# Optimization experiments

Hardware: AMD Instinct MI355X
Metric: run time of the kernel (lower is better)

## Reference

```python
import jax, jax.numpy as jnp
import numpy as np

GAMMA, LMBD, EPS = 0.99, 0.95, 0.2
T, D, H, A = 262144, 128, 256, 8


def _mlp_gauss(x, W1, b1, Wmu, bmu, Wlv, blv):
    h = jnp.tanh(x @ W1 + b1)
    return h @ Wmu + bmu, h @ Wlv + blv  # mu, logvar: [T, A]


def _critic(x, Wc1, bc1, Wc2, bc2):
    h = jnp.tanh(x @ Wc1 + bc1)
    return h @ Wc2 + bc2  # [T, 1]


def setup_inputs() -> dict:
    key = jax.random.key(0)
    ks = jax.random.split(key, 12)
    s = 0.05  # small init scale for stable exp()/ratio
    return {
        "state": jax.random.normal(ks[0], (T, D), jnp.float32),
        "next_state": jax.random.normal(ks[1], (T, D), jnp.float32),
        "action": jax.random.normal(ks[2], (T, A), jnp.float32),
        "beta_log_prob": jax.random.normal(ks[3], (T, A), jnp.float32) * 0.1,
        "reward": jax.random.normal(ks[4], (T,), jnp.float32),
        "W1": jax.random.normal(ks[5], (D, H), jnp.float32) * s,
        "b1": jnp.zeros((H,), jnp.float32),
        "Wmu": jax.random.normal(ks[6], (H, A), jnp.float32) * s,
        "bmu": jnp.zeros((A,), jnp.float32),
        "Wlv": jax.random.normal(ks[7], (H, A), jnp.float32) * s,
        "blv": jnp.zeros((A,), jnp.float32),
        "Wc1": jax.random.normal(ks[8], (D, H), jnp.float32) * s,
        "bc1": jnp.zeros((H,), jnp.float32),
        "Wc2": jax.random.normal(ks[9], (H, 1), jnp.float32) * s,
        "bc2": jnp.zeros((1,), jnp.float32),
    }


def reference(state, next_state, action, beta_log_prob, reward,
              W1, b1, Wmu, bmu, Wlv, blv, Wc1, bc1, Wc2, bc2):
    # critic values
    value = _critic(state, Wc1, bc1, Wc2, bc2)            # [T, 1]
    v0 = value[:, 0]                                       # [T]
    v1 = _critic(next_state, Wc1, bc1, Wc2, bc2)[:, 0]     # [T]

    # GAE: reverse recurrence gae_t = delta_t + gamma*lambda*gae_{t+1}
    delta = reward + GAMMA * v1 - v0                       # [T]

    def step(g, d):
        g = d + GAMMA * LMBD * g
        return g, g

    _, gae_rev = jax.lax.scan(step, jnp.float32(0.0), delta[::-1])
    # torch code rebuilds each gae into a fresh Tensor -> returns are detached
    ret = jax.lax.stop_gradient(gae_rev[::-1][:, None])    # [T, 1]

    advantage = ret - value                                # [T, 1] (grad via value)
    a_hat = (advantage - advantage.mean()) / (jnp.std(advantage, ddof=1) + 1e-7)

    # pi log-prob of actions under Normal(mu, sqrt(exp(logvar)))
    mu, logvar = _mlp_gauss(state, W1, b1, Wmu, bmu, Wlv, blv)  # [T, A]
    log_2pi = jnp.float32(np.log(2.0 * np.pi))
    pi_lp = -0.5 * ((action - mu) ** 2) * jnp.exp(-logvar) - 0.5 * logvar - 0.5 * log_2pi

    ratio = jnp.exp(jnp.sum(pi_lp - jax.lax.stop_gradient(beta_log_prob),
                            axis=1, keepdims=True))        # [T, 1]

    actor_loss = -jnp.sum(jnp.minimum(ratio * a_hat,
                                      jnp.clip(ratio, 1.0 - EPS, 1.0 + EPS) * a_hat))
    critic_loss = jnp.sum(advantage ** 2)
    return actor_loss + critic_loss
```

## Files before the change

### kernel.cpp

```cpp
#include <hip/hip_runtime.h>

#define T_N   262144
#define D_IN  128
#define H_HID 256
#define A_DIM 8
#define GAMMA 0.99f
#define LMBD  0.95f
#define EPS_C 0.2f
#define C_GL  0.9405f
#define W16C  0.37474927f
#define CHUNK 4096
#define NCHUNK 64
#define HALF_LOG_2PI 0.9189385332f

typedef __attribute__((ext_vector_type(8))) short short8;
typedef __attribute__((ext_vector_type(4))) float f32x4;

__device__ __forceinline__ unsigned short f2bf(float f) {
  unsigned int u = __float_as_uint(f);
  u += 0x7FFFu + ((u >> 16) & 1u);
  return (unsigned short)(u >> 16);
}
__device__ __forceinline__ float bf2f(unsigned short h) {
  return __uint_as_float(((unsigned int)h) << 16);
}
__device__ __forceinline__ float fast_tanh(float x) {
  x = fminf(10.f, fmaxf(-10.f, x));
  float e = __expf(2.f * x);
  return 1.f - 2.f * __builtin_amdgcn_rcpf(e + 1.f);
}

__global__ __launch_bounds__(256) void k_prep(
    const float* __restrict__ Wc1, const float* __restrict__ W1,
    const float* __restrict__ Wc2, const float* __restrict__ Wmu,
    const float* __restrict__ Wlv,
    unsigned short* __restrict__ Wc1T, unsigned short* __restrict__ W1T,
    unsigned short* __restrict__ H0, unsigned short* __restrict__ H1) {
  int i = blockIdx.x * 256 + threadIdx.x;
  if (i < 32768) {
    int n = i >> 7, k = i & 127;
    Wc1T[i] = f2bf(Wc1[k * 256 + n]);
  } else if (i < 65536) {
    int j = i - 32768; int n = j >> 7, k = j & 127;
    W1T[j] = f2bf(W1[k * 256 + n]);
  } else if (i < 69632) {
    int j = i - 65536; int h = j >> 8, n = j & 255;
    H0[j] = (h == 0) ? f2bf(Wc2[n]) : (unsigned short)0;
  } else if (i < 73728) {
    int j = i - 69632; int h = j >> 8, n = j & 255;
    H1[j] = (h < 8) ? f2bf(Wmu[n * 8 + h]) : f2bf(Wlv[n * 8 + (h - 8)]);
  }
}

__global__ __launch_bounds__(256) void k_main(
    const float* __restrict__ state, const float* __restrict__ next_state,
    const float* __restrict__ action, const float* __restrict__ beta_lp,
    const unsigned short* __restrict__ Wc1T, const unsigned short* __restrict__ W1T,
    const unsigned short* __restrict__ H0, const unsigned short* __restrict__ H1,
    const float* __restrict__ bc1, const float* __restrict__ b1,
    const float* __restrict__ bc2, const float* __restrict__ bmu,
    const float* __restrict__ blv,
    float* __restrict__ v0out, float* __restrict__ v1out,
    float* __restrict__ ratio) {
  const int job = blockIdx.y;
  const int r0  = blockIdx.x * 64;
  const int tid = threadIdx.x;
  const int lane = tid & 63;
  const int wv   = tid >> 6;
  const int c    = lane & 15;
  const int quad = lane >> 4;

  __shared__ unsigned short sh_x[64 * 136];
  __shared__ unsigned short sh_h[64 * 264];
  __shared__ unsigned short sh_wh[16 * 264];
  __shared__ float sh_hb[64 * 16];

  const float* X = (job == 1) ? next_state : state;
  const unsigned short* WT = (job == 2) ? W1T : Wc1T;
  const float* bias = (job == 2) ? b1 : bc1;
  const unsigned short* HW = (job == 2) ? H1 : H0;

  {
    const float4* Xv = (const float4*)(X + r0 * D_IN);
#pragma unroll
    for (int it = 0; it < 8; ++it) {
      int f4 = tid + it * 256;
      int row = f4 >> 5, c4 = f4 & 31;
      float4 v = Xv[f4];
      ushort4 u;
      u.x = f2bf(v.x); u.y = f2bf(v.y); u.z = f2bf(v.z); u.w = f2bf(v.w);
      *(ushort4*)(&sh_x[row * 136 + c4 * 4]) = u;
    }
#pragma unroll
    for (int it = 0; it < 16; ++it) {
      int j = tid + it * 256;
      sh_wh[(j >> 8) * 264 + (j & 255)] = HW[j];
    }
  }
  __syncthreads();

  short8 bfrag[4][4];
  float bias_c[4];
#pragma unroll
  for (int ct = 0; ct < 4; ++ct) {
    int n = wv * 64 + ct * 16 + c;
    bias_c[ct] = bias[n];
#pragma unroll
    for (int ki = 0; ki < 4; ++ki)
      bfrag[ct][ki] = *(const short8*)(WT + n * 128 + ki * 32 + quad * 8);
  }

#pragma unroll
  for (int rt = 0; rt < 4; ++rt) {
    f32x4 acc[4];
#pragma unroll
    for (int ct = 0; ct < 4; ++ct) acc[ct] = (f32x4){0.f, 0.f, 0.f, 0.f};
#pragma unroll
    for (int ki = 0; ki < 4; ++ki) {
      short8 a = *(const short8*)(&sh_x[(rt * 16 + c) * 136 + ki * 32 + quad * 8]);
#pragma unroll
      for (int ct = 0; ct < 4; ++ct)
        acc[ct] = __builtin_amdgcn_mfma_f32_16x16x32_bf16(a, bfrag[ct][ki], acc[ct], 0, 0, 0);
    }
#pragma unroll
    for (int ct = 0; ct < 4; ++ct) {
      int col = wv * 64 + ct * 16 + c;
#pragma unroll
      for (int r = 0; r < 4; ++r) {
        int row = rt * 16 + quad * 4 + r;
        sh_h[row * 264 + col] = f2bf(fast_tanh(acc[ct][r] + bias_c[ct]));
      }
    }
  }
  __syncthreads();

  {
    f32x4 acc2 = (f32x4){0.f, 0.f, 0.f, 0.f};
#pragma unroll
    for (int ki = 0; ki < 8; ++ki) {
      short8 a2 = *(const short8*)(&sh_wh[c * 264 + ki * 32 + quad * 8]);
      short8 b2 = *(const short8*)(&sh_h[(wv * 16 + c) * 264 + ki * 32 + quad * 8]);
      acc2 = __builtin_amdgcn_mfma_f32_16x16x32_bf16(a2, b2, acc2, 0, 0, 0);
    }
    *((f32x4*)&sh_hb[(wv * 16 + c) * 16 + quad * 4]) = acc2;
  }
  __syncthreads();

  if (tid < 64) {
    int s = tid, t = r0 + s;
    if (job == 0) {
      v0out[t] = sh_hb[s * 16] + bc2[0];
    } else if (job == 1) {
      v1out[t] = sh_hb[s * 16] + bc2[0];
    } else {
      float slp = 0.f;
#pragma unroll
      for (int a = 0; a < A_DIM; ++a) {
        float mu = sh_hb[s * 16 + a] + bmu[a];
        float lv = sh_hb[s * 16 + 8 + a] + blv[a];
        float ac = action[t * A_DIM + a];
        float bl = beta_lp[t * A_DIM + a];
        float d = ac - mu;
        slp += -0.5f * d * d * __expf(-lv) - 0.5f * lv - HALF_LOG_2PI - bl;
      }
      ratio[t] = __expf(slp);
    }
  }
}

__global__ __launch_bounds__(256) void k_delta(
    const float* __restrict__ reward, const float* __restrict__ v0,
    const float* __restrict__ v1, float* __restrict__ delta,
    float* __restrict__ chunkS) {
  int j = blockIdx.x, k = threadIdx.x;
  int base = j * CHUNK + k * 16;
  float s = 0.f, wgt = 1.f;
#pragma unroll
  for (int i = 0; i < 16; ++i) {
    float d = reward[base + i] + GAMMA * v1[base + i] - v0[base + i];
    delta[base + i] = d;
    s += wgt * d;
    wgt *= C_GL;
  }
  __shared__ float red[256];
  red[k] = __powf(W16C, (float)k) * s;
  __syncthreads();
  for (int off = 128; off > 0; off >>= 1) {
    if (k < off) red[k] += red[k + off];
    __syncthreads();
  }
  if (k == 0) chunkS[j] = red[0];
}

__global__ void k_carry(const float* __restrict__ chunkS, float* __restrict__ carry) {
  if (threadIdx.x == 0) {
    float g = 0.f;
    for (int j = NCHUNK - 1; j >= 0; --j) {
      carry[j] = g;
      g = chunkS[j] + 0.0f * g;
    }
  }
}

__global__ __launch_bounds__(256) void k_gae(
    const float* __restrict__ delta, const float* __restrict__ value,
    const float* __restrict__ carry, float* __restrict__ adv,
    float* __restrict__ accs) {
  int j = blockIdx.x, k = threadIdx.x;
  int base = j * CHUNK + k * 16;
  float d[16];
  float s = 0.f, wgt = 1.f;
#pragma unroll
  for (int i = 0; i < 16; ++i) {
    d[i] = delta[base + i];
    s += wgt * d[i];
    wgt *= C_GL;
  }
  __shared__ float Ss[256], Sw[256];
  Ss[k] = s; Sw[k] = W16C;
  __syncthreads();
  for (int dd = 1; dd < 256; dd <<= 1) {
    bool has = (k + dd) < 256;
    float ns = 0.f, nw = 0.f;
    if (has) { ns = Ss[k] + Sw[k] * Ss[k + dd]; nw = Sw[k] * Sw[k + dd]; }
    __syncthreads();
    if (has) { Ss[k] = ns; Sw[k] = nw; }
    __syncthreads();
  }
  float g = ((k < 255) ? Ss[k + 1] : 0.f) + __powf(W16C, (float)(255 - k)) * carry[j];
  float sa = 0.f, sq = 0.f;
#pragma unroll
  for (int i = 15; i >= 0; --i) {
    g = d[i] + C_GL * g;
    float a = g - value[base + i];
    adv[base + i] = a;
    sa += a; sq += a * a;
  }
  __syncthreads();
  Ss[k] = sa; Sw[k] = sq;
  __syncthreads();
  for (int off = 128; off > 0; off >>= 1) {
    if (k < off) { Ss[k] += Ss[k + off]; Sw[k] += Sw[k + off]; }
    __syncthreads();
  }
  if (k == 0) {
    atomicAdd(&accs[0], Ss[0]);
    atomicAdd(&accs[1], Sw[0]);
  }
}

__global__ __launch_bounds__(256) void k_actor(
    const float* __restrict__ adv, const float* __restrict__ ratio,
    float* __restrict__ accs) {
  int t = blockIdx.x * 256 + threadIdx.x;
  float sum  = accs[0];
  float mean = sum * (1.f / (float)T_N);
  float var  = (accs[1] - sum * mean) / (float)(T_N - 1);
  float inv  = 1.f / (sqrtf(var) + 1e-7f);
  float a = (adv[t] - mean) * inv;
  float r = ratio[t];
  float rc = fminf(fmaxf(r, 1.f - EPS_C), 1.f + EPS_C);
  float term = -fminf(r * a, rc * a);
  __shared__ float red[256];
  int k = threadIdx.x;
  red[k] = term;
  __syncthreads();
  for (int off = 128; off > 0; off >>= 1) {
    if (k < off) red[k] += red[k + off];
    __syncthreads();
  }
  if (k == 0) atomicAdd(&accs[2], red[0]);
}

__global__ void k_fin(const float* __restrict__ accs, float* __restrict__ out) {
  out[0] = accs[2] + accs[1];
}

extern "C" void kernel_launch(void* const* d_in, const int* in_sizes, int n_in,
                              void* d_out, int out_size, void* d_ws, size_t ws_size,
                              hipStream_t stream) {
  const float* state      = (const float*)d_in[0];
  const float* next_state = (const float*)d_in[1];
  const float* action     = (const float*)d_in[2];
  const float* beta_lp    = (const float*)d_in[3];
  const float* reward     = (const float*)d_in[4];
  const float* W1   = (const float*)d_in[5];
  const float* b1   = (const float*)d_in[6];
  const float* Wmu  = (const float*)d_in[7];
  const float* bmu  = (const float*)d_in[8];
  const float* Wlv  = (const float*)d_in[9];
  const float* blv  = (const float*)d_in[10];
  const float* Wc1  = (const float*)d_in[11];
  const float* bc1  = (const float*)d_in[12];
  const float* Wc2  = (const float*)d_in[13];
  const float* bc2  = (const float*)d_in[14];

  char* ws = (char*)d_ws;
  size_t o = 0;
  unsigned short* Wc1T = (unsigned short*)(ws + o); o += 65536;
  unsigned short* W1T  = (unsigned short*)(ws + o); o += 65536;
  unsigned short* H0   = (unsigned short*)(ws + o); o += 8192;
  unsigned short* H1   = (unsigned short*)(ws + o); o += 8192;
  float* v0    = (float*)(ws + o); o += (size_t)T_N * 4;
  float* v1    = (float*)(ws + o); o += (size_t)T_N * 4;
  float* ratio = (float*)(ws + o); o += (size_t)T_N * 4;
  float* delta = (float*)(ws + o); o += (size_t)T_N * 4;
  float* adv   = (float*)(ws + o); o += (size_t)T_N * 4;
  float* chunkS = (float*)(ws + o); o += 256;
  float* carry  = (float*)(ws + o); o += 256;
  float* accs   = (float*)(ws + o); o += 256;

  hipMemsetAsync(accs, 0, 16, stream);

  k_prep<<<288, 256, 0, stream>>>(Wc1, W1, Wc2, Wmu, Wlv, Wc1T, W1T, H0, H1);

  dim3 gmain(T_N / 64, 3);
  k_main<<<gmain, 256, 0, stream>>>(state, next_state, action, beta_lp,
                                    Wc1T, W1T, H0, H1, bc1, b1, bc2, bmu, blv,
                                    v0, v1, ratio);

  k_delta<<<NCHUNK, 256, 0, stream>>>(reward, v0, v1, delta, chunkS);
  k_carry<<<1, 64, 0, stream>>>(chunkS, carry);
  k_gae<<<NCHUNK, 256, 0, stream>>>(delta, v0, carry, adv, accs);
  k_actor<<<T_N / 256, 256, 0, stream>>>(adv, ratio, accs);
  k_fin<<<1, 1, 0, stream>>>(accs, (float*)d_out);
}
```

Baseline: 437.7 us.

## Split critic/actor kernels, fuse critic output layer, single-pass overlapping-window GAE

```diff
diff --git a/kernel.cpp b/kernel.cpp
--- a/kernel.cpp
+++ b/kernel.cpp
@@ -5,12 +5,8 @@
 #define H_HID 256
 #define A_DIM 8
 #define GAMMA 0.99f
-#define LMBD  0.95f
 #define EPS_C 0.2f
 #define C_GL  0.9405f
-#define W16C  0.37474927f
-#define CHUNK 4096
-#define NCHUNK 64
 #define HALF_LOG_2PI 0.9189385332f
 
 typedef __attribute__((ext_vector_type(8))) short short8;
@@ -21,9 +17,6 @@
   u += 0x7FFFu + ((u >> 16) & 1u);
   return (unsigned short)(u >> 16);
 }
-__device__ __forceinline__ float bf2f(unsigned short h) {
-  return __uint_as_float(((unsigned int)h) << 16);
-}
 __device__ __forceinline__ float fast_tanh(float x) {
   x = fminf(10.f, fmaxf(-10.f, x));
   float e = __expf(2.f * x);
@@ -32,10 +25,9 @@
 
 __global__ __launch_bounds__(256) void k_prep(
     const float* __restrict__ Wc1, const float* __restrict__ W1,
-    const float* __restrict__ Wc2, const float* __restrict__ Wmu,
-    const float* __restrict__ Wlv,
+    const float* __restrict__ Wmu, const float* __restrict__ Wlv,
     unsigned short* __restrict__ Wc1T, unsigned short* __restrict__ W1T,
-    unsigned short* __restrict__ H0, unsigned short* __restrict__ H1) {
+    unsigned short* __restrict__ H1) {
   int i = blockIdx.x * 256 + threadIdx.x;
   if (i < 32768) {
     int n = i >> 7, k = i & 127;
@@ -45,23 +37,16 @@
     W1T[j] = f2bf(W1[k * 256 + n]);
   } else if (i < 69632) {
     int j = i - 65536; int h = j >> 8, n = j & 255;
-    H0[j] = (h == 0) ? f2bf(Wc2[n]) : (unsigned short)0;
-  } else if (i < 73728) {
-    int j = i - 69632; int h = j >> 8, n = j & 255;
     H1[j] = (h < 8) ? f2bf(Wmu[n * 8 + h]) : f2bf(Wlv[n * 8 + (h - 8)]);
   }
 }
 
-__global__ __launch_bounds__(256) void k_main(
+__global__ __launch_bounds__(256, 4) void k_critic(
     const float* __restrict__ state, const float* __restrict__ next_state,
-    const float* __restrict__ action, const float* __restrict__ beta_lp,
-    const unsigned short* __restrict__ Wc1T, const unsigned short* __restrict__ W1T,
-    const unsigned short* __restrict__ H0, const unsigned short* __restrict__ H1,
-    const float* __restrict__ bc1, const float* __restrict__ b1,
-    const float* __restrict__ bc2, const float* __restrict__ bmu,
-    const float* __restrict__ blv,
-    float* __restrict__ v0out, float* __restrict__ v1out,
-    float* __restrict__ ratio) {
+    const unsigned short* __restrict__ Wc1T,
+    const float* __restrict__ bc1, const float* __restrict__ Wc2,
+    const float* __restrict__ bc2,
+    float* __restrict__ v0out, float* __restrict__ v1out) {
   const int job = blockIdx.y;
   const int r0  = blockIdx.x * 64;
   const int tid = threadIdx.x;
@@ -71,14 +56,10 @@
   const int quad = lane >> 4;
 
   __shared__ unsigned short sh_x[64 * 136];
-  __shared__ unsigned short sh_h[64 * 264];
-  __shared__ unsigned short sh_wh[16 * 264];
-  __shared__ float sh_hb[64 * 16];
-
-  const float* X = (job == 1) ? next_state : state;
-  const unsigned short* WT = (job == 2) ? W1T : Wc1T;
-  const float* bias = (job == 2) ? b1 : bc1;
-  const unsigned short* HW = (job == 2) ? H1 : H0;
+  __shared__ float sh_v[64 * 4];
+
+  const float* X = job ? next_state : state;
+  float* out = job ? v1out : v0out;
 
   {
     const float4* Xv = (const float4*)(X + r0 * D_IN);
@@ -91,27 +72,98 @@
       u.x = f2bf(v.x); u.y = f2bf(v.y); u.z = f2bf(v.z); u.w = f2bf(v.w);
       *(ushort4*)(&sh_x[row * 136 + c4 * 4]) = u;
     }
-#pragma unroll
-    for (int it = 0; it < 16; ++it) {
-      int j = tid + it * 256;
-      sh_wh[(j >> 8) * 264 + (j & 255)] = HW[j];
-    }
-  }
-  __syncthreads();
+  }
+
+  short8 bfrag[4][4];
+  float bias_c[4], wc2_c[4];
+#pragma unroll
+  for (int ct = 0; ct < 4; ++ct) {
+    int n = wv * 64 + ct * 16 + c;
+    bias_c[ct] = bc1[n];
+    wc2_c[ct]  = Wc2[n];
+#pragma unroll
+    for (int ki = 0; ki < 4; ++ki)
+      bfrag[ct][ki] = *(const short8*)(Wc1T + n * 128 + ki * 32 + quad * 8);
+  }
+  __syncthreads();
+
+#pragma unroll
+  for (int rt = 0; rt < 4; ++rt) {
+    f32x4 acc[4];
+#pragma unroll
+    for (int ct = 0; ct < 4; ++ct) acc[ct] = (f32x4){0.f, 0.f, 0.f, 0.f};
+#pragma unroll
+    for (int ki = 0; ki < 4; ++ki) {
+      short8 a = *(const short8*)(&sh_x[(rt * 16 + c) * 136 + ki * 32 + quad * 8]);
+#pragma unroll
+      for (int ct = 0; ct < 4; ++ct)
+        acc[ct] = __builtin_amdgcn_mfma_f32_16x16x32_bf16(a, bfrag[ct][ki], acc[ct], 0, 0, 0);
+    }
+#pragma unroll
+    for (int r = 0; r < 4; ++r) {
+      float p = 0.f;
+#pragma unroll
+      for (int ct = 0; ct < 4; ++ct)
+        p += fast_tanh(acc[ct][r] + bias_c[ct]) * wc2_c[ct];
+      p += __shfl_xor(p, 1);
+      p += __shfl_xor(p, 2);
+      p += __shfl_xor(p, 4);
+      p += __shfl_xor(p, 8);
+      if (c == 0) sh_v[(rt * 16 + quad * 4 + r) * 4 + wv] = p;
+    }
+  }
+  __syncthreads();
+  if (tid < 64) {
+    out[r0 + tid] = sh_v[tid * 4] + sh_v[tid * 4 + 1] + sh_v[tid * 4 + 2] +
+                    sh_v[tid * 4 + 3] + bc2[0];
+  }
+}
+
+__global__ __launch_bounds__(256, 4) void k_actor(
+    const float* __restrict__ state,
+    const float* __restrict__ action, const float* __restrict__ beta_lp,
+    const unsigned short* __restrict__ W1T, const unsigned short* __restrict__ H1,
+    const float* __restrict__ b1, const float* __restrict__ bmu,
+    const float* __restrict__ blv,
+    float* __restrict__ ratio) {
+  const int r0  = blockIdx.x * 32;
+  const int tid = threadIdx.x;
+  const int lane = tid & 63;
+  const int wv   = tid >> 6;
+  const int c    = lane & 15;
+  const int quad = lane >> 4;
+
+  __shared__ unsigned short sh_x[32 * 136];
+  __shared__ unsigned short sh_h[32 * 264];
+  __shared__ float sh_hb[2 * 32 * 16];
+
+  {
+    const float4* Xv = (const float4*)(state + r0 * D_IN);
+#pragma unroll
+    for (int it = 0; it < 4; ++it) {
+      int f4 = tid + it * 256;
+      int row = f4 >> 5, c4 = f4 & 31;
+      float4 v = Xv[f4];
+      ushort4 u;
+      u.x = f2bf(v.x); u.y = f2bf(v.y); u.z = f2bf(v.z); u.w = f2bf(v.w);
+      *(ushort4*)(&sh_x[row * 136 + c4 * 4]) = u;
+    }
+  }
 
   short8 bfrag[4][4];
   float bias_c[4];
 #pragma unroll
   for (int ct = 0; ct < 4; ++ct) {
     int n = wv * 64 + ct * 16 + c;
-    bias_c[ct] = bias[n];
+    bias_c[ct] = b1[n];
 #pragma unroll
     for (int ki = 0; ki < 4; ++ki)
-      bfrag[ct][ki] = *(const short8*)(WT + n * 128 + ki * 32 + quad * 8);
-  }
-
-#pragma unroll
-  for (int rt = 0; rt < 4; ++rt) {
+      bfrag[ct][ki] = *(const short8*)(W1T + n * 128 + ki * 32 + quad * 8);
+  }
+  __syncthreads();
+
+#pragma unroll
+  for (int rt = 0; rt < 2; ++rt) {
     f32x4 acc[4];
 #pragma unroll
     for (int ct = 0; ct < 4; ++ct) acc[ct] = (f32x4){0.f, 0.f, 0.f, 0.f};
@@ -135,89 +187,56 @@
   __syncthreads();
 
   {
+    const int st = wv & 1;
+    const int kh = wv >> 1;
     f32x4 acc2 = (f32x4){0.f, 0.f, 0.f, 0.f};
 #pragma unroll
-    for (int ki = 0; ki < 8; ++ki) {
-      short8 a2 = *(const short8*)(&sh_wh[c * 264 + ki * 32 + quad * 8]);
-      short8 b2 = *(const short8*)(&sh_h[(wv * 16 + c) * 264 + ki * 32 + quad * 8]);
+    for (int kk = 0; kk < 4; ++kk) {
+      int ki = kh * 4 + kk;
+      short8 a2 = *(const short8*)(H1 + c * 256 + ki * 32 + quad * 8);
+      short8 b2 = *(const short8*)(&sh_h[(st * 16 + c) * 264 + ki * 32 + quad * 8]);
       acc2 = __builtin_amdgcn_mfma_f32_16x16x32_bf16(a2, b2, acc2, 0, 0, 0);
     }
-    *((f32x4*)&sh_hb[(wv * 16 + c) * 16 + quad * 4]) = acc2;
-  }
-  __syncthreads();
-
-  if (tid < 64) {
-    int s = tid, t = r0 + s;
-    if (job == 0) {
-      v0out[t] = sh_hb[s * 16] + bc2[0];
-    } else if (job == 1) {
-      v1out[t] = sh_hb[s * 16] + bc2[0];
-    } else {
-      float slp = 0.f;
-#pragma unroll
-      for (int a = 0; a < A_DIM; ++a) {
-        float mu = sh_hb[s * 16 + a] + bmu[a];
-        float lv = sh_hb[s * 16 + 8 + a] + blv[a];
-        float ac = action[t * A_DIM + a];
-        float bl = beta_lp[t * A_DIM + a];
-        float d = ac - mu;
-        slp += -0.5f * d * d * __expf(-lv) - 0.5f * lv - HALF_LOG_2PI - bl;
-      }
-      ratio[t] = __expf(slp);
-    }
-  }
-}
-
-__global__ __launch_bounds__(256) void k_delta(
+    *((f32x4*)&sh_hb[(kh * 32 + st * 16 + c) * 16 + quad * 4]) = acc2;
+  }
+  __syncthreads();
+
+  {
+    int s = tid >> 3, a = tid & 7;
+    int t = r0 + s;
+    float mu = sh_hb[(s)*16 + a] + sh_hb[(32 + s) * 16 + a] + bmu[a];
+    float lv = sh_hb[(s)*16 + 8 + a] + sh_hb[(32 + s) * 16 + 8 + a] + blv[a];
+    float ac = action[t * A_DIM + a];
+    float bl = beta_lp[t * A_DIM + a];
+    float d = ac - mu;
+    float term = -0.5f * d * d * __expf(-lv) - 0.5f * lv - HALF_LOG_2PI - bl;
+    term += __shfl_xor(term, 1);
+    term += __shfl_xor(term, 2);
+    term += __shfl_xor(term, 4);
+    if (a == 0) ratio[t] = __expf(term);
+  }
+}
+
+__global__ __launch_bounds__(256) void k_gae(
     const float* __restrict__ reward, const float* __restrict__ v0,
-    const float* __restrict__ v1, float* __restrict__ delta,
-    float* __restrict__ chunkS) {
-  int j = blockIdx.x, k = threadIdx.x;
-  int base = j * CHUNK + k * 16;
-  float s = 0.f, wgt = 1.f;
-#pragma unroll
-  for (int i = 0; i < 16; ++i) {
-    float d = reward[base + i] + GAMMA * v1[base + i] - v0[base + i];
-    delta[base + i] = d;
-    s += wgt * d;
-    wgt *= C_GL;
-  }
-  __shared__ float red[256];
-  red[k] = __powf(W16C, (float)k) * s;
-  __syncthreads();
-  for (int off = 128; off > 0; off >>= 1) {
-    if (k < off) red[k] += red[k + off];
-    __syncthreads();
-  }
-  if (k == 0) chunkS[j] = red[0];
-}
-
-__global__ void k_carry(const float* __restrict__ chunkS, float* __restrict__ carry) {
-  if (threadIdx.x == 0) {
-    float g = 0.f;
-    for (int j = NCHUNK - 1; j >= 0; --j) {
-      carry[j] = g;
-      g = chunkS[j] + 0.0f * g;
-    }
-  }
-}
-
-__global__ __launch_bounds__(256) void k_gae(
-    const float* __restrict__ delta, const float* __restrict__ value,
-    const float* __restrict__ carry, float* __restrict__ adv,
+    const float* __restrict__ v1, float* __restrict__ adv,
     float* __restrict__ accs) {
-  int j = blockIdx.x, k = threadIdx.x;
-  int base = j * CHUNK + k * 16;
-  float d[16];
-  float s = 0.f, wgt = 1.f;
-#pragma unroll
-  for (int i = 0; i < 16; ++i) {
-    d[i] = delta[base + i];
-    s += wgt * d[i];
-    wgt *= C_GL;
-  }
+  const int j = blockIdx.x, k = threadIdx.x;
+  const int base = j * 1024 + k * 8;
+  float d[8];
+  float s = 0.f, w = 1.f;
+#pragma unroll
+  for (int i = 0; i < 8; ++i) {
+    int idx = base + i;
+    float dd = 0.f;
+    if (idx < T_N) dd = reward[idx] + GAMMA * v1[idx] - v0[idx];
+    d[i] = dd;
+    s += w * dd;
+    w *= C_GL;
+  }
+  const float W8 = w;
   __shared__ float Ss[256], Sw[256];
-  Ss[k] = s; Sw[k] = W16C;
+  Ss[k] = s; Sw[k] = W8;
   __syncthreads();
   for (int dd = 1; dd < 256; dd <<= 1) {
     bool has = (k + dd) < 256;
@@ -227,14 +246,16 @@
     if (has) { Ss[k] = ns; Sw[k] = nw; }
     __syncthreads();
   }
-  float g = ((k < 255) ? Ss[k + 1] : 0.f) + __powf(W16C, (float)(255 - k)) * carry[j];
+  float g = (k < 255) ? Ss[k + 1] : 0.f;
   float sa = 0.f, sq = 0.f;
-#pragma unroll
-  for (int i = 15; i >= 0; --i) {
-    g = d[i] + C_GL * g;
-    float a = g - value[base + i];
-    adv[base + i] = a;
-    sa += a; sq += a * a;
+  if (k < 128) {
+#pragma unroll
+    for (int i = 7; i >= 0; --i) {
+      g = d[i] + C_GL * g;
+      float a = g - v0[base + i];
+      adv[base + i] = a;
+      sa += a; sq += a * a;
+    }
   }
   __syncthreads();
   Ss[k] = sa; Sw[k] = sq;
@@ -249,7 +270,7 @@
   }
 }
 
-__global__ __launch_bounds__(256) void k_actor(
+__global__ __launch_bounds__(256) void k_loss(
     const float* __restrict__ adv, const float* __restrict__ ratio,
     float* __restrict__ accs) {
   int t = blockIdx.x * 256 + threadIdx.x;
@@ -299,29 +320,23 @@
   size_t o = 0;
   unsigned short* Wc1T = (unsigned short*)(ws + o); o += 65536;
   unsigned short* W1T  = (unsigned short*)(ws + o); o += 65536;
-  unsigned short* H0   = (unsigned short*)(ws + o); o += 8192;
   unsigned short* H1   = (unsigned short*)(ws + o); o += 8192;
   float* v0    = (float*)(ws + o); o += (size_t)T_N * 4;
   float* v1    = (float*)(ws + o); o += (size_t)T_N * 4;
   float* ratio = (float*)(ws + o); o += (size_t)T_N * 4;
-  float* delta = (float*)(ws + o); o += (size_t)T_N * 4;
   float* adv   = (float*)(ws + o); o += (size_t)T_N * 4;
-  float* chunkS = (float*)(ws + o); o += 256;
-  float* carry  = (float*)(ws + o); o += 256;
-  float* accs   = (float*)(ws + o); o += 256;
+  float* accs  = (float*)(ws + o); o += 256;
 
   hipMemsetAsync(accs, 0, 16, stream);
 
-  k_prep<<<288, 256, 0, stream>>>(Wc1, W1, Wc2, Wmu, Wlv, Wc1T, W1T, H0, H1);
-
-  dim3 gmain(T_N / 64, 3);
-  k_main<<<gmain, 256, 0, stream>>>(state, next_state, action, beta_lp,
-                                    Wc1T, W1T, H0, H1, bc1, b1, bc2, bmu, blv,
-                                    v0, v1, ratio);
-
-  k_delta<<<NCHUNK, 256, 0, stream>>>(reward, v0, v1, delta, chunkS);
-  k_carry<<<1, 64, 0, stream>>>(chunkS, carry);
-  k_gae<<<NCHUNK, 256, 0, stream>>>(delta, v0, carry, adv, accs);
-  k_actor<<<T_N / 256, 256, 0, stream>>>(adv, ratio, accs);
+  k_prep<<<272, 256, 0, stream>>>(Wc1, W1, Wmu, Wlv, Wc1T, W1T, H1);
+
+  dim3 gcrit(T_N / 64, 2);
+  k_critic<<<gcrit, 256, 0, stream>>>(state, next_state, Wc1T, bc1, Wc2, bc2,
+                                      v0, v1);
+  k_actor<<<T_N / 32, 256, 0, stream>>>(state, action, beta_lp, W1T, H1,
+                                        b1, bmu, blv, ratio);
+  k_gae<<<256, 256, 0, stream>>>(reward, v0, v1, adv, accs);
+  k_loss<<<T_N / 256, 256, 0, stream>>>(adv, ratio, accs);
   k_fin<<<1, 1, 0, stream>>>(accs, (float*)d_out);
 }
```

After: 440.4 us. About the same (+0.6%).
